# Kernel optimization log

Measured on AMD Instinct MI355X. Metric: run time of the kernel, lower is better.

## Reference

```python
import jax, jax.numpy as jnp
import numpy as np

N_NODES = 50000
N_HEDGES = 100000
E = 800000          # node->node incidences and hedge->node incidences
F_IN = 128
F_H = 64
F_OUT = 128


def setup_inputs() -> dict:
    key = jax.random.key(0)
    ks = jax.random.split(key, 10)
    node_features = jax.random.normal(ks[0], (N_NODES, F_IN), jnp.float32)
    hedge_features = jax.random.normal(ks[1], (N_HEDGES, F_H), jnp.float32)
    node_senders = jax.random.randint(ks[2], (E,), 0, N_NODES)
    node_receivers = jnp.sort(jax.random.randint(ks[3], (E,), 0, N_NODES))
    node_convolution = jax.random.uniform(ks[4], (E, 1), jnp.float32)
    hedge2node_senders = jax.random.randint(ks[5], (E,), 0, N_HEDGES)
    hedge2node_receivers = jnp.sort(jax.random.randint(ks[6], (E,), 0, N_NODES))
    hedge2node_convolution = jax.random.uniform(ks[7], (E, 1), jnp.float32)
    # eqx.nn.Linear-style uniform init: U(-1/sqrt(fan_in), 1/sqrt(fan_in))
    lim1 = 1.0 / np.sqrt(F_IN)
    lim2 = 1.0 / np.sqrt(F_H)
    W_msg = jax.random.uniform(ks[8], (F_OUT, F_IN), jnp.float32, -lim1, lim1)
    b_msg = jnp.zeros((F_OUT,), jnp.float32)
    W_scale = jax.random.uniform(ks[9], (F_OUT, F_H), jnp.float32, -lim2, lim2)
    b_scale = jnp.zeros((F_OUT,), jnp.float32)
    return dict(node_features=node_features, hedge_features=hedge_features,
                node_senders=node_senders, node_receivers=node_receivers,
                node_convolution=node_convolution,
                hedge2node_senders=hedge2node_senders,
                hedge2node_receivers=hedge2node_receivers,
                hedge2node_convolution=hedge2node_convolution,
                W_msg=W_msg, b_msg=b_msg, W_scale=W_scale, b_scale=b_scale)


def reference(node_features, hedge_features, node_senders, node_receivers,
              node_convolution, hedge2node_senders, hedge2node_receivers,
              hedge2node_convolution, W_msg, b_msg, W_scale, b_scale):
    # pipeline 1: gather node senders -> linear -> scale -> scatter-add to receivers
    sender_features = node_features[node_senders]                 # [E, F_IN]
    messages = sender_features @ W_msg.T + b_msg                  # [E, F_OUT]
    gathered_messages = jax.ops.segment_sum(
        node_convolution * messages, node_receivers, num_segments=N_NODES)
    # pipeline 2: gather hedge senders -> linear -> scale -> scatter-add to receivers
    hedge_sender_features = hedge_features[hedge2node_senders]    # [E, F_H]
    hedge_messages = hedge_sender_features @ W_scale.T + b_scale  # [E, F_OUT]
    gathered_scaling = jax.ops.segment_sum(
        hedge2node_convolution * hedge_messages, hedge2node_receivers,
        num_segments=N_NODES)
    return jnp.tanh(gathered_scaling * gathered_messages)         # [N_NODES, F_OUT]
```

## Files before the change

kernel.cpp:

```cpp
#include <hip/hip_runtime.h>

#define N_NODES   50000
#define N_HEDGES  100000
#define E_EDGES   800000
#define F_IN      128
#define F_H       64
#define F_OUT     128

typedef __attribute__((ext_vector_type(8))) short short8;
typedef __attribute__((ext_vector_type(4))) float f32x4;
typedef _Float16 half2_t __attribute__((ext_vector_type(2)));
typedef _Float16 half4_t __attribute__((ext_vector_type(4)));

__device__ __forceinline__ unsigned short f2bf(float f) {
    unsigned int u = __float_as_uint(f);
    return (unsigned short)((u + 0x7fffu + ((u >> 16) & 1u)) >> 16);
}
__device__ __forceinline__ float bf2f(unsigned short h) {
    return __uint_as_float(((unsigned int)h) << 16);
}

#define OFF_ITEMS (2 * (N_NODES + 1) + F_OUT * (F_IN + F_H))
#define OFF_B     ((OFF_ITEMS + 255) / 256)
#define CONV_NODE_F4  (N_NODES * 32)
#define CONV_HEDGE_F4 (N_HEDGES * 16)
#define CONV_B    ((CONV_NODE_F4 + CONV_HEDGE_F4 + 255) / 256)

__global__ __launch_bounds__(256)
void offsets_kernel(const int* __restrict__ recv1, const int* __restrict__ recv2,
                    int* __restrict__ offs1, int* __restrict__ offs2,
                    const float* __restrict__ Wm, const float* __restrict__ Wsc,
                    unsigned short* __restrict__ wmhi, unsigned short* __restrict__ wmlo,
                    unsigned short* __restrict__ wshi, unsigned short* __restrict__ wslo,
                    const float* __restrict__ nf, const float* __restrict__ hf,
                    _Float16* __restrict__ nfH, _Float16* __restrict__ hfH) {
    if (blockIdx.x < OFF_B) {
        int t = blockIdx.x * blockDim.x + threadIdx.x;
        const int total = N_NODES + 1;
        if (t < total) {
            int r = t, lo = 0, hi = E_EDGES;
            while (lo < hi) { int mid = (lo + hi) >> 1; if (recv1[mid] < r) lo = mid + 1; else hi = mid; }
            offs1[r] = lo;
        } else if (t < 2 * total) {
            int r = t - total, lo = 0, hi = E_EDGES;
            while (lo < hi) { int mid = (lo + hi) >> 1; if (recv2[mid] < r) lo = mid + 1; else hi = mid; }
            offs2[r] = lo;
        } else if (t < OFF_ITEMS) {
            int idx = t - 2 * total;
            if (idx < F_OUT * F_IN) {
                float f = Wm[idx];
                unsigned short h = f2bf(f);
                wmhi[idx] = h; wmlo[idx] = f2bf(f - bf2f(h));
            } else {
                int i2 = idx - F_OUT * F_IN;
                float f = Wsc[i2];
                unsigned short h = f2bf(f);
                wshi[i2] = h; wslo[i2] = f2bf(f - bf2f(h));
            }
        }
    } else {
        int idx = (blockIdx.x - OFF_B) * 256 + threadIdx.x;
        if (idx < CONV_NODE_F4) {
            float4 v = *(const float4*)(nf + (size_t)idx * 4);
            half4_t h = { (_Float16)v.x, (_Float16)v.y, (_Float16)v.z, (_Float16)v.w };
            *(half4_t*)(nfH + (size_t)idx * 4) = h;
        } else {
            int i2 = idx - CONV_NODE_F4;
            if (i2 < CONV_HEDGE_F4) {
                float4 v = *(const float4*)(hf + (size_t)i2 * 4);
                half4_t h = { (_Float16)v.x, (_Float16)v.y, (_Float16)v.z, (_Float16)v.w };
                *(half4_t*)(hfH + (size_t)i2 * 4) = h;
            }
        }
    }
}

__global__ __launch_bounds__(256)
void gather_fused(const _Float16* __restrict__ nfH, const _Float16* __restrict__ hfH,
                  const int* __restrict__ snd1, const float* __restrict__ cv1,
                  const int* __restrict__ o1,
                  const int* __restrict__ snd2, const float* __restrict__ cv2,
                  const int* __restrict__ o2,
                  char* a1pack, char* __restrict__ a2pack,
                  float* __restrict__ cs1o, float* __restrict__ cs2o) {
    const int lane = threadIdx.x & 63;
    const int wid  = threadIdx.x >> 6;

    if (blockIdx.x < N_NODES / 4) {
        const int node = blockIdx.x * 4 + wid;
        const int s = o1[node], e = o1[node + 1];
        float a0 = 0.f, a1 = 0.f, b0 = 0.f, b1 = 0.f, csA = 0.f, csB = 0.f;
        const _Float16* base = nfH + lane * 2;
        int i = s;
        for (; i + 8 <= e; i += 8) {
            int   s0 = snd1[i],   s1 = snd1[i+1], s2 = snd1[i+2], s3 = snd1[i+3];
            int   s4 = snd1[i+4], s5 = snd1[i+5], s6 = snd1[i+6], s7 = snd1[i+7];
            float c0 = cv1[i],    c1 = cv1[i+1],  c2 = cv1[i+2],  c3 = cv1[i+3];
            float c4 = cv1[i+4],  c5 = cv1[i+5],  c6 = cv1[i+6],  c7 = cv1[i+7];
            half2_t v0 = *(const half2_t*)(base + (size_t)s0 * F_IN);
            half2_t v1 = *(const half2_t*)(base + (size_t)s1 * F_IN);
            half2_t v2 = *(const half2_t*)(base + (size_t)s2 * F_IN);
            half2_t v3 = *(const half2_t*)(base + (size_t)s3 * F_IN);
            half2_t v4 = *(const half2_t*)(base + (size_t)s4 * F_IN);
            half2_t v5 = *(const half2_t*)(base + (size_t)s5 * F_IN);
            half2_t v6 = *(const half2_t*)(base + (size_t)s6 * F_IN);
            half2_t v7 = *(const half2_t*)(base + (size_t)s7 * F_IN);
            a0 += c0 * (float)v0.x; a1 += c0 * (float)v0.y;
            a0 += c1 * (float)v1.x; a1 += c1 * (float)v1.y;
            a0 += c2 * (float)v2.x; a1 += c2 * (float)v2.y;
            a0 += c3 * (float)v3.x; a1 += c3 * (float)v3.y;
            b0 += c4 * (float)v4.x; b1 += c4 * (float)v4.y;
            b0 += c5 * (float)v5.x; b1 += c5 * (float)v5.y;
            b0 += c6 * (float)v6.x; b1 += c6 * (float)v6.y;
            b0 += c7 * (float)v7.x; b1 += c7 * (float)v7.y;
            csA += c0 + c1 + c2 + c3; csB += c4 + c5 + c6 + c7;
        }
        for (; i + 4 <= e; i += 4) {
            int   s0 = snd1[i],   s1 = snd1[i+1], s2 = snd1[i+2], s3 = snd1[i+3];
            float c0 = cv1[i],    c1 = cv1[i+1],  c2 = cv1[i+2],  c3 = cv1[i+3];
            half2_t v0 = *(const half2_t*)(base + (size_t)s0 * F_IN);
            half2_t v1 = *(const half2_t*)(base + (size_t)s1 * F_IN);
            half2_t v2 = *(const half2_t*)(base + (size_t)s2 * F_IN);
            half2_t v3 = *(const half2_t*)(base + (size_t)s3 * F_IN);
            a0 += c0 * (float)v0.x; a1 += c0 * (float)v0.y;
            a0 += c1 * (float)v1.x; a1 += c1 * (float)v1.y;
            b0 += c2 * (float)v2.x; b1 += c2 * (float)v2.y;
            b0 += c3 * (float)v3.x; b1 += c3 * (float)v3.y;
            csA += c0 + c1; csB += c2 + c3;
        }
        for (; i < e; ++i) {
            int sn = snd1[i]; float c = cv1[i];
            half2_t v = *(const half2_t*)(base + (size_t)sn * F_IN);
            a0 += c * (float)v.x; a1 += c * (float)v.y; csA += c;
        }
        a0 += b0; a1 += b1;
        float cs = csA + csB;
        unsigned short h0 = f2bf(a0), h1 = f2bf(a1);
        unsigned short l0 = f2bf(a0 - bf2f(h0)), l1 = f2bf(a1 - bf2f(h1));
        unsigned int* hp = (unsigned int*)(a1pack + (size_t)node * 512);
        unsigned int* lp = (unsigned int*)(a1pack + (size_t)node * 512 + 256);
        hp[lane] = (unsigned int)h0 | ((unsigned int)h1 << 16);
        lp[lane] = (unsigned int)l0 | ((unsigned int)l1 << 16);
        if (lane == 0) cs1o[node] = cs;
    } else {
        const int node = (blockIdx.x - N_NODES / 4) * 4 + wid;
        const int s = o2[node], e = o2[node + 1];
        float a = 0.f, b = 0.f, csA = 0.f, csB = 0.f;
        const _Float16* base = hfH + lane;
        int i = s;
        for (; i + 8 <= e; i += 8) {
            int   s0 = snd2[i],   s1 = snd2[i+1], s2 = snd2[i+2], s3 = snd2[i+3];
            int   s4 = snd2[i+4], s5 = snd2[i+5], s6 = snd2[i+6], s7 = snd2[i+7];
            float c0 = cv2[i],    c1 = cv2[i+1],  c2 = cv2[i+2],  c3 = cv2[i+3];
            float c4 = cv2[i+4],  c5 = cv2[i+5],  c6 = cv2[i+6],  c7 = cv2[i+7];
            float v0 = (float)base[(size_t)s0 * F_H], v1 = (float)base[(size_t)s1 * F_H];
            float v2 = (float)base[(size_t)s2 * F_H], v3 = (float)base[(size_t)s3 * F_H];
            float v4 = (float)base[(size_t)s4 * F_H], v5 = (float)base[(size_t)s5 * F_H];
            float v6 = (float)base[(size_t)s6 * F_H], v7 = (float)base[(size_t)s7 * F_H];
            a += c0 * v0; a += c1 * v1; a += c2 * v2; a += c3 * v3;
            b += c4 * v4; b += c5 * v5; b += c6 * v6; b += c7 * v7;
            csA += c0 + c1 + c2 + c3; csB += c4 + c5 + c6 + c7;
        }
        for (; i + 4 <= e; i += 4) {
            int   s0 = snd2[i],   s1 = snd2[i+1], s2 = snd2[i+2], s3 = snd2[i+3];
            float c0 = cv2[i],    c1 = cv2[i+1],  c2 = cv2[i+2],  c3 = cv2[i+3];
            float v0 = (float)base[(size_t)s0 * F_H], v1 = (float)base[(size_t)s1 * F_H];
            float v2 = (float)base[(size_t)s2 * F_H], v3 = (float)base[(size_t)s3 * F_H];
            a += c0 * v0; a += c1 * v1; b += c2 * v2; b += c3 * v3;
            csA += c0 + c1; csB += c2 + c3;
        }
        for (; i < e; ++i) {
            int sn = snd2[i]; float c = cv2[i];
            a += c * (float)base[(size_t)sn * F_H]; csA += c;
        }
        a += b;
        float cs = csA + csB;
        unsigned short h = f2bf(a);
        unsigned short l = f2bf(a - bf2f(h));
        ((unsigned short*)(a2pack + (size_t)node * 256))[lane]       = h;
        ((unsigned short*)(a2pack + (size_t)node * 256 + 128))[lane] = l;
        if (lane == 0) cs2o[node] = cs;
    }
}

__global__ __launch_bounds__(256)
void gather_nodes_kernel(const float* __restrict__ nf, const int* __restrict__ senders,
                         const float* __restrict__ conv, const int* __restrict__ offs,
                         char* a1pack, float* __restrict__ csum_out) {
    const int lane = threadIdx.x & 63;
    const int node = blockIdx.x * 4 + (threadIdx.x >> 6);
    const int s = offs[node], e = offs[node + 1];
    float a0 = 0.f, a1 = 0.f, cs = 0.f;
    const float* base = nf + lane * 2;
    int i = s;
    for (; i + 4 <= e; i += 4) {
        int   s0 = senders[i],   s1 = senders[i+1], s2 = senders[i+2], s3 = senders[i+3];
        float c0 = conv[i],      c1 = conv[i+1],    c2 = conv[i+2],    c3 = conv[i+3];
        float2 v0 = *(const float2*)(base + s0 * F_IN);
        float2 v1 = *(const float2*)(base + s1 * F_IN);
        float2 v2 = *(const float2*)(base + s2 * F_IN);
        float2 v3 = *(const float2*)(base + s3 * F_IN);
        a0 += c0 * v0.x; a1 += c0 * v0.y;
        a0 += c1 * v1.x; a1 += c1 * v1.y;
        a0 += c2 * v2.x; a1 += c2 * v2.y;
        a0 += c3 * v3.x; a1 += c3 * v3.y;
        cs += c0 + c1 + c2 + c3;
    }
    for (; i < e; ++i) {
        int sn = senders[i]; float c = conv[i];
        float2 v = *(const float2*)(base + sn * F_IN);
        a0 += c * v.x; a1 += c * v.y; cs += c;
    }
    unsigned short h0 = f2bf(a0), h1 = f2bf(a1);
    unsigned short l0 = f2bf(a0 - bf2f(h0)), l1 = f2bf(a1 - bf2f(h1));
    unsigned int* hp = (unsigned int*)(a1pack + (size_t)node * 512);
    unsigned int* lp = (unsigned int*)(a1pack + (size_t)node * 512 + 256);
    hp[lane] = (unsigned int)h0 | ((unsigned int)h1 << 16);
    lp[lane] = (unsigned int)l0 | ((unsigned int)l1 << 16);
    if (lane == 0) csum_out[node] = cs;
}

__global__ __launch_bounds__(256)
void gather_hedges_kernel(const float* __restrict__ hf, const int* __restrict__ senders,
                          const float* __restrict__ conv, const int* __restrict__ offs,
                          char* __restrict__ a2pack, float* __restrict__ csum_out) {
    const int lane = threadIdx.x & 63;
    const int node = blockIdx.x * 4 + (threadIdx.x >> 6);
    const int s = offs[node], e = offs[node + 1];
    float a = 0.f, cs = 0.f;
    const float* base = hf + lane;
    int i = s;
    for (; i + 4 <= e; i += 4) {
        int   s0 = senders[i],   s1 = senders[i+1], s2 = senders[i+2], s3 = senders[i+3];
        float c0 = conv[i],      c1 = conv[i+1],    c2 = conv[i+2],    c3 = conv[i+3];
        float v0 = base[s0 * F_H], v1 = base[s1 * F_H];
        float v2 = base[s2 * F_H], v3 = base[s3 * F_H];
        a += c0 * v0; a += c1 * v1; a += c2 * v2; a += c3 * v3;
        cs += c0 + c1 + c2 + c3;
    }
    for (; i < e; ++i) {
        int sn = senders[i]; float c = conv[i];
        a += c * base[sn * F_H]; cs += c;
    }
    unsigned short h = f2bf(a);
    unsigned short l = f2bf(a - bf2f(h));
    ((unsigned short*)(a2pack + (size_t)node * 256))[lane]       = h;
    ((unsigned short*)(a2pack + (size_t)node * 256 + 128))[lane] = l;
    if (lane == 0) csum_out[node] = cs;
}

__global__ __launch_bounds__(256)
void gemm_tanh_kernel(const char* a1pack,
                      const char* __restrict__ a2pack,
                      const float* __restrict__ csum1, const float* __restrict__ csum2,
                      const unsigned short* __restrict__ wmhi, const unsigned short* __restrict__ wmlo,
                      const unsigned short* __restrict__ wshi, const unsigned short* __restrict__ wslo,
                      const float* __restrict__ bm, const float* __restrict__ bs,
                      float* outp) {
    __shared__ __align__(16) char sA1[16 * 512];
    __shared__ __align__(16) char sA2[16 * 256];
    __shared__ float sCs[16][2];

    const int t   = threadIdx.x;
    const int wid = t >> 6;
    const int l   = t & 63;
    const int g   = l >> 4;
    const int jl  = l & 15;

    short8 wm_h[2][4], wm_l[2][4], ws_h[2][2], ws_l[2][2];
    float bmj[2], bsj[2];
    #pragma unroll
    for (int jt = 0; jt < 2; ++jt) {
        const int j = wid * 32 + jt * 16 + jl;
        #pragma unroll
        for (int ks = 0; ks < 4; ++ks) {
            wm_h[jt][ks] = *(const short8*)(wmhi + j * F_IN + ks * 32 + g * 8);
            wm_l[jt][ks] = *(const short8*)(wmlo + j * F_IN + ks * 32 + g * 8);
        }
        #pragma unroll
        for (int ks = 0; ks < 2; ++ks) {
            ws_h[jt][ks] = *(const short8*)(wshi + j * F_H + ks * 32 + g * 8);
            ws_l[jt][ks] = *(const short8*)(wslo + j * F_H + ks * 32 + g * 8);
        }
        bmj[jt] = bm[j]; bsj[jt] = bs[j];
    }

    #pragma unroll 1
    for (int ns = 0; ns < 4; ++ns) {
        const int n0 = blockIdx.x * 64 + ns * 16;
        #pragma unroll
        for (int it = 0; it < 2; ++it) {
            int fi = (it << 8) + t;
            int ci = fi & 31, row = fi >> 5;
            int nsrc = min(n0 + row, N_NODES - 1);
            float4 v = *(const float4*)(a1pack + (size_t)nsrc * 512 + ci * 16);
            *(float4*)(sA1 + row * 512 + (((unsigned)ci << 4) ^ (((unsigned)row & 7) << 4))) = v;
        }
        {
            int ci = t & 15, row = t >> 4;
            int nsrc = min(n0 + row, N_NODES - 1);
            float4 v = *(const float4*)(a2pack + (size_t)nsrc * 256 + ci * 16);
            *(float4*)(sA2 + row * 256 + (((unsigned)ci << 4) ^ (((unsigned)row & 7) << 4))) = v;
        }
        if (t < 16)      sCs[t][0]      = csum1[min(n0 + t, N_NODES - 1)];
        else if (t < 32) sCs[t - 16][1] = csum2[min(n0 + t - 16, N_NODES - 1)];
        __syncthreads();

        short8 a1h[4], a1l[4], a2h[2], a2l[2];
        const unsigned sw = ((unsigned)jl & 7) << 4;
        #pragma unroll
        for (int ks = 0; ks < 4; ++ks) {
            unsigned cc = (((unsigned)(4 * ks + g)) << 4) ^ sw;
            a1h[ks] = *(const short8*)(sA1 + jl * 512 + cc);
            a1l[ks] = *(const short8*)(sA1 + jl * 512 + 256 + cc);
        }
        #pragma unroll
        for (int ks = 0; ks < 2; ++ks) {
            unsigned cc = (((unsigned)(4 * ks + g)) << 4) ^ sw;
            a2h[ks] = *(const short8*)(sA2 + jl * 256 + cc);
            a2l[ks] = *(const short8*)(sA2 + jl * 256 + 128 + cc);
        }

        #pragma unroll
        for (int jt = 0; jt < 2; ++jt) {
            f32x4 c1 = {0.f, 0.f, 0.f, 0.f}, c2 = {0.f, 0.f, 0.f, 0.f};
            #pragma unroll
            for (int ks = 0; ks < 4; ++ks) {
                c1 = __builtin_amdgcn_mfma_f32_16x16x32_bf16(a1h[ks], wm_h[jt][ks], c1, 0, 0, 0);
                c1 = __builtin_amdgcn_mfma_f32_16x16x32_bf16(a1h[ks], wm_l[jt][ks], c1, 0, 0, 0);
                c1 = __builtin_amdgcn_mfma_f32_16x16x32_bf16(a1l[ks], wm_h[jt][ks], c1, 0, 0, 0);
            }
            #pragma unroll
            for (int ks = 0; ks < 2; ++ks) {
                c2 = __builtin_amdgcn_mfma_f32_16x16x32_bf16(a2h[ks], ws_h[jt][ks], c2, 0, 0, 0);
                c2 = __builtin_amdgcn_mfma_f32_16x16x32_bf16(a2h[ks], ws_l[jt][ks], c2, 0, 0, 0);
                c2 = __builtin_amdgcn_mfma_f32_16x16x32_bf16(a2l[ks], ws_h[jt][ks], c2, 0, 0, 0);
            }
            const int j = wid * 32 + jt * 16 + jl;
            #pragma unroll
            for (int r = 0; r < 4; ++r) {
                int row  = g * 4 + r;
                int node = n0 + row;
                if (node < N_NODES) {
                    float v1 = c1[r] + sCs[row][0] * bmj[jt];
                    float v2 = c2[r] + sCs[row][1] * bsj[jt];
                    outp[(size_t)node * F_OUT + j] = tanhf(v1 * v2);
                }
            }
        }
        __syncthreads();
    }
}

extern "C" void kernel_launch(void* const* d_in, const int* in_sizes, int n_in,
                              void* d_out, int out_size, void* d_ws, size_t ws_size,
                              hipStream_t stream) {
    const float* node_features  = (const float*)d_in[0];
    const float* hedge_features = (const float*)d_in[1];
    const int*   node_senders   = (const int*)d_in[2];
    const int*   node_receivers = (const int*)d_in[3];
    const float* node_conv      = (const float*)d_in[4];
    const int*   h2n_senders    = (const int*)d_in[5];
    const int*   h2n_receivers  = (const int*)d_in[6];
    const float* h2n_conv       = (const float*)d_in[7];
    const float* W_msg          = (const float*)d_in[8];
    const float* b_msg          = (const float*)d_in[9];
    const float* W_scale        = (const float*)d_in[10];
    const float* b_scale        = (const float*)d_in[11];

    float* out = (float*)d_out;
    char*  ws  = (char*)d_ws;

    char*  A2pack = ws;
    float* Csum1  = (float*)(ws + 12800000);
    float* Csum2  = (float*)(ws + 13000000);
    int*   offs1  = (int*)  (ws + 13200000);
    int*   offs2  = (int*)  (ws + 13400016);
    unsigned short* wmhi = (unsigned short*)(ws + 13600032);
    unsigned short* wmlo = (unsigned short*)(ws + 13632800);
    unsigned short* wshi = (unsigned short*)(ws + 13665568);
    unsigned short* wslo = (unsigned short*)(ws + 13681952);
    _Float16* nfH = (_Float16*)(ws + 13698560);
    _Float16* hfH = (_Float16*)(ws + 26498560);
    const size_t WS_NEED_FAST = 39298560;
    char*  A1pack = (char*)d_out;

    const bool fast = (ws_size >= WS_NEED_FAST);

    if (fast) {
        offsets_kernel<<<OFF_B + CONV_B, 256, 0, stream>>>(
            node_receivers, h2n_receivers, offs1, offs2,
            W_msg, W_scale, wmhi, wmlo, wshi, wslo,
            node_features, hedge_features, nfH, hfH);
        gather_fused<<<2 * (N_NODES / 4), 256, 0, stream>>>(
            nfH, hfH,
            node_senders, node_conv, offs1,
            h2n_senders, h2n_conv, offs2,
            A1pack, A2pack, Csum1, Csum2);
    } else {
        offsets_kernel<<<OFF_B, 256, 0, stream>>>(
            node_receivers, h2n_receivers, offs1, offs2,
            W_msg, W_scale, wmhi, wmlo, wshi, wslo,
            node_features, hedge_features, nfH, hfH);
        gather_nodes_kernel<<<N_NODES / 4, 256, 0, stream>>>(
            node_features, node_senders, node_conv, offs1, A1pack, Csum1);
        gather_hedges_kernel<<<N_NODES / 4, 256, 0, stream>>>(
            hedge_features, h2n_senders, h2n_conv, offs2, A2pack, Csum2);
    }

    gemm_tanh_kernel<<<(N_NODES + 63) / 64, 256, 0, stream>>>(
        A1pack, A2pack, Csum1, Csum2, wmhi, wmlo, wshi, wslo,
        b_msg, b_scale, out);
}
```

Before: 113.3 us.

## Fuse segment gathers with MFMA GEMM and tanh in one kernel

Result: slower. 132.7 us (+17.2%).

```diff
diff --git a/kernel.cpp b/kernel.cpp
--- a/kernel.cpp
+++ b/kernel.cpp
@@ -75,19 +75,26 @@
     }
 }
 
-__global__ __launch_bounds__(256)
-void gather_fused(const _Float16* __restrict__ nfH, const _Float16* __restrict__ hfH,
-                  const int* __restrict__ snd1, const float* __restrict__ cv1,
-                  const int* __restrict__ o1,
-                  const int* __restrict__ snd2, const float* __restrict__ cv2,
-                  const int* __restrict__ o2,
-                  char* a1pack, char* __restrict__ a2pack,
-                  float* __restrict__ cs1o, float* __restrict__ cs2o) {
-    const int lane = threadIdx.x & 63;
-    const int wid  = threadIdx.x >> 6;
-
-    if (blockIdx.x < N_NODES / 4) {
-        const int node = blockIdx.x * 4 + wid;
+__global__ __launch_bounds__(1024)
+void fused_gather_gemm(const _Float16* __restrict__ nfH, const _Float16* __restrict__ hfH,
+                       const int* __restrict__ snd1, const float* __restrict__ cv1,
+                       const int* __restrict__ o1,
+                       const int* __restrict__ snd2, const float* __restrict__ cv2,
+                       const int* __restrict__ o2,
+                       const unsigned short* __restrict__ wmhi, const unsigned short* __restrict__ wmlo,
+                       const unsigned short* __restrict__ wshi, const unsigned short* __restrict__ wslo,
+                       const float* __restrict__ bm, const float* __restrict__ bs,
+                       float* __restrict__ outp) {
+    __shared__ __align__(16) char sA1[16 * 512];
+    __shared__ __align__(16) char sA2[16 * 256];
+    __shared__ float sCs[16][2];
+
+    const int t    = threadIdx.x;
+    const int wid  = t >> 6;
+    const int lane = t & 63;
+    const int node = blockIdx.x * 16 + wid;
+
+    {
         const int s = o1[node], e = o1[node + 1];
         float a0 = 0.f, a1 = 0.f, b0 = 0.f, b1 = 0.f, csA = 0.f, csB = 0.f;
         const _Float16* base = nfH + lane * 2;
@@ -134,16 +141,17 @@
             a0 += c * (float)v.x; a1 += c * (float)v.y; csA += c;
         }
         a0 += b0; a1 += b1;
-        float cs = csA + csB;
         unsigned short h0 = f2bf(a0), h1 = f2bf(a1);
         unsigned short l0 = f2bf(a0 - bf2f(h0)), l1 = f2bf(a1 - bf2f(h1));
-        unsigned int* hp = (unsigned int*)(a1pack + (size_t)node * 512);
-        unsigned int* lp = (unsigned int*)(a1pack + (size_t)node * 512 + 256);
-        hp[lane] = (unsigned int)h0 | ((unsigned int)h1 << 16);
-        lp[lane] = (unsigned int)l0 | ((unsigned int)l1 << 16);
-        if (lane == 0) cs1o[node] = cs;
-    } else {
-        const int node = (blockIdx.x - N_NODES / 4) * 4 + wid;
+        unsigned int hi = (unsigned int)h0 | ((unsigned int)h1 << 16);
+        unsigned int lo = (unsigned int)l0 | ((unsigned int)l1 << 16);
+        unsigned off = ((unsigned)(lane * 4)) ^ (((unsigned)wid & 7) << 4);
+        *(unsigned int*)(sA1 + wid * 512 + off)       = hi;
+        *(unsigned int*)(sA1 + wid * 512 + 256 + off) = lo;
+        if (lane == 0) sCs[wid][0] = csA + csB;
+    }
+
+    {
         const int s = o2[node], e = o2[node + 1];
         float a = 0.f, b = 0.f, csA = 0.f, csB = 0.f;
         const _Float16* base = hfH + lane;
@@ -174,181 +182,62 @@
             a += c * (float)base[(size_t)sn * F_H]; csA += c;
         }
         a += b;
-        float cs = csA + csB;
         unsigned short h = f2bf(a);
         unsigned short l = f2bf(a - bf2f(h));
-        ((unsigned short*)(a2pack + (size_t)node * 256))[lane]       = h;
-        ((unsigned short*)(a2pack + (size_t)node * 256 + 128))[lane] = l;
-        if (lane == 0) cs2o[node] = cs;
-    }
-}
-
-__global__ __launch_bounds__(256)
-void gather_nodes_kernel(const float* __restrict__ nf, const int* __restrict__ senders,
-                         const float* __restrict__ conv, const int* __restrict__ offs,
-                         char* a1pack, float* __restrict__ csum_out) {
-    const int lane = threadIdx.x & 63;
-    const int node = blockIdx.x * 4 + (threadIdx.x >> 6);
-    const int s = offs[node], e = offs[node + 1];
-    float a0 = 0.f, a1 = 0.f, cs = 0.f;
-    const float* base = nf + lane * 2;
-    int i = s;
-    for (; i + 4 <= e; i += 4) {
-        int   s0 = senders[i],   s1 = senders[i+1], s2 = senders[i+2], s3 = senders[i+3];
-        float c0 = conv[i],      c1 = conv[i+1],    c2 = conv[i+2],    c3 = conv[i+3];
-        float2 v0 = *(const float2*)(base + s0 * F_IN);
-        float2 v1 = *(const float2*)(base + s1 * F_IN);
-        float2 v2 = *(const float2*)(base + s2 * F_IN);
-        float2 v3 = *(const float2*)(base + s3 * F_IN);
-        a0 += c0 * v0.x; a1 += c0 * v0.y;
-        a0 += c1 * v1.x; a1 += c1 * v1.y;
-        a0 += c2 * v2.x; a1 += c2 * v2.y;
-        a0 += c3 * v3.x; a1 += c3 * v3.y;
-        cs += c0 + c1 + c2 + c3;
-    }
-    for (; i < e; ++i) {
-        int sn = senders[i]; float c = conv[i];
-        float2 v = *(const float2*)(base + sn * F_IN);
-        a0 += c * v.x; a1 += c * v.y; cs += c;
-    }
-    unsigned short h0 = f2bf(a0), h1 = f2bf(a1);
-    unsigned short l0 = f2bf(a0 - bf2f(h0)), l1 = f2bf(a1 - bf2f(h1));
-    unsigned int* hp = (unsigned int*)(a1pack + (size_t)node * 512);
-    unsigned int* lp = (unsigned int*)(a1pack + (size_t)node * 512 + 256);
-    hp[lane] = (unsigned int)h0 | ((unsigned int)h1 << 16);
-    lp[lane] = (unsigned int)l0 | ((unsigned int)l1 << 16);
-    if (lane == 0) csum_out[node] = cs;
-}
-
-__global__ __launch_bounds__(256)
-void gather_hedges_kernel(const float* __restrict__ hf, const int* __restrict__ senders,
-                          const float* __restrict__ conv, const int* __restrict__ offs,
-                          char* __restrict__ a2pack, float* __restrict__ csum_out) {
-    const int lane = threadIdx.x & 63;
-    const int node = blockIdx.x * 4 + (threadIdx.x >> 6);
-    const int s = offs[node], e = offs[node + 1];
-    float a = 0.f, cs = 0.f;
-    const float* base = hf + lane;
-    int i = s;
-    for (; i + 4 <= e; i += 4) {
-        int   s0 = senders[i],   s1 = senders[i+1], s2 = senders[i+2], s3 = senders[i+3];
-        float c0 = conv[i],      c1 = conv[i+1],    c2 = conv[i+2],    c3 = conv[i+3];
-        float v0 = base[s0 * F_H], v1 = base[s1 * F_H];
-        float v2 = base[s2 * F_H], v3 = base[s3 * F_H];
-        a += c0 * v0; a += c1 * v1; a += c2 * v2; a += c3 * v3;
-        cs += c0 + c1 + c2 + c3;
-    }
-    for (; i < e; ++i) {
-        int sn = senders[i]; float c = conv[i];
-        a += c * base[sn * F_H]; cs += c;
-    }
-    unsigned short h = f2bf(a);
-    unsigned short l = f2bf(a - bf2f(h));
-    ((unsigned short*)(a2pack + (size_t)node * 256))[lane]       = h;
-    ((unsigned short*)(a2pack + (size_t)node * 256 + 128))[lane] = l;
-    if (lane == 0) csum_out[node] = cs;
-}
-
-__global__ __launch_bounds__(256)
-void gemm_tanh_kernel(const char* a1pack,
-                      const char* __restrict__ a2pack,
-                      const float* __restrict__ csum1, const float* __restrict__ csum2,
-                      const unsigned short* __restrict__ wmhi, const unsigned short* __restrict__ wmlo,
-                      const unsigned short* __restrict__ wshi, const unsigned short* __restrict__ wslo,
-                      const float* __restrict__ bm, const float* __restrict__ bs,
-                      float* outp) {
-    __shared__ __align__(16) char sA1[16 * 512];
-    __shared__ __align__(16) char sA2[16 * 256];
-    __shared__ float sCs[16][2];
-
-    const int t   = threadIdx.x;
-    const int wid = t >> 6;
-    const int l   = t & 63;
-    const int g   = l >> 4;
-    const int jl  = l & 15;
-
-    short8 wm_h[2][4], wm_l[2][4], ws_h[2][2], ws_l[2][2];
-    float bmj[2], bsj[2];
-    #pragma unroll
-    for (int jt = 0; jt < 2; ++jt) {
-        const int j = wid * 32 + jt * 16 + jl;
-        #pragma unroll
-        for (int ks = 0; ks < 4; ++ks) {
-            wm_h[jt][ks] = *(const short8*)(wmhi + j * F_IN + ks * 32 + g * 8);
-            wm_l[jt][ks] = *(const short8*)(wmlo + j * F_IN + ks * 32 + g * 8);
-        }
-        #pragma unroll
-        for (int ks = 0; ks < 2; ++ks) {
-            ws_h[jt][ks] = *(const short8*)(wshi + j * F_H + ks * 32 + g * 8);
-            ws_l[jt][ks] = *(const short8*)(wslo + j * F_H + ks * 32 + g * 8);
-        }
-        bmj[jt] = bm[j]; bsj[jt] = bs[j];
-    }
-
-    #pragma unroll 1
-    for (int ns = 0; ns < 4; ++ns) {
-        const int n0 = blockIdx.x * 64 + ns * 16;
-        #pragma unroll
-        for (int it = 0; it < 2; ++it) {
-            int fi = (it << 8) + t;
-            int ci = fi & 31, row = fi >> 5;
-            int nsrc = min(n0 + row, N_NODES - 1);
-            float4 v = *(const float4*)(a1pack + (size_t)nsrc * 512 + ci * 16);
-            *(float4*)(sA1 + row * 512 + (((unsigned)ci << 4) ^ (((unsigned)row & 7) << 4))) = v;
-        }
-        {
-            int ci = t & 15, row = t >> 4;
-            int nsrc = min(n0 + row, N_NODES - 1);
-            float4 v = *(const float4*)(a2pack + (size_t)nsrc * 256 + ci * 16);
-            *(float4*)(sA2 + row * 256 + (((unsigned)ci << 4) ^ (((unsigned)row & 7) << 4))) = v;
-        }
-        if (t < 16)      sCs[t][0]      = csum1[min(n0 + t, N_NODES - 1)];
-        else if (t < 32) sCs[t - 16][1] = csum2[min(n0 + t - 16, N_NODES - 1)];
-        __syncthreads();
-
-        short8 a1h[4], a1l[4], a2h[2], a2l[2];
-        const unsigned sw = ((unsigned)jl & 7) << 4;
-        #pragma unroll
-        for (int ks = 0; ks < 4; ++ks) {
-            unsigned cc = (((unsigned)(4 * ks + g)) << 4) ^ sw;
-            a1h[ks] = *(const short8*)(sA1 + jl * 512 + cc);
-            a1l[ks] = *(const short8*)(sA1 + jl * 512 + 256 + cc);
-        }
-        #pragma unroll
-        for (int ks = 0; ks < 2; ++ks) {
-            unsigned cc = (((unsigned)(4 * ks + g)) << 4) ^ sw;
-            a2h[ks] = *(const short8*)(sA2 + jl * 256 + cc);
-            a2l[ks] = *(const short8*)(sA2 + jl * 256 + 128 + cc);
-        }
-
-        #pragma unroll
-        for (int jt = 0; jt < 2; ++jt) {
-            f32x4 c1 = {0.f, 0.f, 0.f, 0.f}, c2 = {0.f, 0.f, 0.f, 0.f};
-            #pragma unroll
-            for (int ks = 0; ks < 4; ++ks) {
-                c1 = __builtin_amdgcn_mfma_f32_16x16x32_bf16(a1h[ks], wm_h[jt][ks], c1, 0, 0, 0);
-                c1 = __builtin_amdgcn_mfma_f32_16x16x32_bf16(a1h[ks], wm_l[jt][ks], c1, 0, 0, 0);
-                c1 = __builtin_amdgcn_mfma_f32_16x16x32_bf16(a1l[ks], wm_h[jt][ks], c1, 0, 0, 0);
-            }
-            #pragma unroll
-            for (int ks = 0; ks < 2; ++ks) {
-                c2 = __builtin_amdgcn_mfma_f32_16x16x32_bf16(a2h[ks], ws_h[jt][ks], c2, 0, 0, 0);
-                c2 = __builtin_amdgcn_mfma_f32_16x16x32_bf16(a2h[ks], ws_l[jt][ks], c2, 0, 0, 0);
-                c2 = __builtin_amdgcn_mfma_f32_16x16x32_bf16(a2l[ks], ws_h[jt][ks], c2, 0, 0, 0);
-            }
-            const int j = wid * 32 + jt * 16 + jl;
-            #pragma unroll
-            for (int r = 0; r < 4; ++r) {
-                int row  = g * 4 + r;
-                int node = n0 + row;
-                if (node < N_NODES) {
-                    float v1 = c1[r] + sCs[row][0] * bmj[jt];
-                    float v2 = c2[r] + sCs[row][1] * bsj[jt];
-                    outp[(size_t)node * F_OUT + j] = tanhf(v1 * v2);
-                }
-            }
-        }
-        __syncthreads();
+        unsigned off = ((unsigned)(lane * 2)) ^ (((unsigned)wid & 7) << 4);
+        *(unsigned short*)(sA2 + wid * 256 + off)       = h;
+        *(unsigned short*)(sA2 + wid * 256 + 128 + off) = l;
+        if (lane == 0) sCs[wid][1] = csA + csB;
+    }
+
+    __syncthreads();
+    if (wid >= 8) return;
+
+    const int g  = lane >> 4;
+    const int jl = lane & 15;
+    const int j  = wid * 16 + jl;
+
+    short8 wm_h[4], wm_l[4], ws_h[2], ws_l[2];
+    #pragma unroll
+    for (int ks = 0; ks < 4; ++ks) {
+        wm_h[ks] = *(const short8*)(wmhi + j * F_IN + ks * 32 + g * 8);
+        wm_l[ks] = *(const short8*)(wmlo + j * F_IN + ks * 32 + g * 8);
+    }
+    #pragma unroll
+    for (int ks = 0; ks < 2; ++ks) {
+        ws_h[ks] = *(const short8*)(wshi + j * F_H + ks * 32 + g * 8);
+        ws_l[ks] = *(const short8*)(wslo + j * F_H + ks * 32 + g * 8);
+    }
+    const float bmj = bm[j], bsj = bs[j];
+
+    const unsigned sw = ((unsigned)jl & 7) << 4;
+    f32x4 c1 = {0.f, 0.f, 0.f, 0.f}, c2 = {0.f, 0.f, 0.f, 0.f};
+    #pragma unroll
+    for (int ks = 0; ks < 4; ++ks) {
+        unsigned cc = (((unsigned)(4 * ks + g)) << 4) ^ sw;
+        short8 a1h = *(const short8*)(sA1 + jl * 512 + cc);
+        short8 a1l = *(const short8*)(sA1 + jl * 512 + 256 + cc);
+        c1 = __builtin_amdgcn_mfma_f32_16x16x32_bf16(a1h, wm_h[ks], c1, 0, 0, 0);
+        c1 = __builtin_amdgcn_mfma_f32_16x16x32_bf16(a1h, wm_l[ks], c1, 0, 0, 0);
+        c1 = __builtin_amdgcn_mfma_f32_16x16x32_bf16(a1l, wm_h[ks], c1, 0, 0, 0);
+    }
+    #pragma unroll
+    for (int ks = 0; ks < 2; ++ks) {
+        unsigned cc = (((unsigned)(4 * ks + g)) << 4) ^ sw;
+        short8 a2h = *(const short8*)(sA2 + jl * 256 + cc);
+        short8 a2l = *(const short8*)(sA2 + jl * 256 + 128 + cc);
+        c2 = __builtin_amdgcn_mfma_f32_16x16x32_bf16(a2h, ws_h[ks], c2, 0, 0, 0);
+        c2 = __builtin_amdgcn_mfma_f32_16x16x32_bf16(a2h, ws_l[ks], c2, 0, 0, 0);
+        c2 = __builtin_amdgcn_mfma_f32_16x16x32_bf16(a2l, ws_h[ks], c2, 0, 0, 0);
+    }
+
+    const int n0 = blockIdx.x * 16;
+    #pragma unroll
+    for (int r = 0; r < 4; ++r) {
+        int row = g * 4 + r;
+        float v1 = c1[r] + sCs[row][0] * bmj;
+        float v2 = c2[r] + sCs[row][1] * bsj;
+        outp[(size_t)(n0 + row) * F_OUT + j] = tanhf(v1 * v2);
     }
 }
 
@@ -371,44 +260,24 @@
     float* out = (float*)d_out;
     char*  ws  = (char*)d_ws;
 
-    char*  A2pack = ws;
-    float* Csum1  = (float*)(ws + 12800000);
-    float* Csum2  = (float*)(ws + 13000000);
-    int*   offs1  = (int*)  (ws + 13200000);
-    int*   offs2  = (int*)  (ws + 13400016);
-    unsigned short* wmhi = (unsigned short*)(ws + 13600032);
-    unsigned short* wmlo = (unsigned short*)(ws + 13632800);
-    unsigned short* wshi = (unsigned short*)(ws + 13665568);
-    unsigned short* wslo = (unsigned short*)(ws + 13681952);
-    _Float16* nfH = (_Float16*)(ws + 13698560);
-    _Float16* hfH = (_Float16*)(ws + 26498560);
-    const size_t WS_NEED_FAST = 39298560;
-    char*  A1pack = (char*)d_out;
-
-    const bool fast = (ws_size >= WS_NEED_FAST);
-
-    if (fast) {
-        offsets_kernel<<<OFF_B + CONV_B, 256, 0, stream>>>(
-            node_receivers, h2n_receivers, offs1, offs2,
-            W_msg, W_scale, wmhi, wmlo, wshi, wslo,
-            node_features, hedge_features, nfH, hfH);
-        gather_fused<<<2 * (N_NODES / 4), 256, 0, stream>>>(
-            nfH, hfH,
-            node_senders, node_conv, offs1,
-            h2n_senders, h2n_conv, offs2,
-            A1pack, A2pack, Csum1, Csum2);
-    } else {
-        offsets_kernel<<<OFF_B, 256, 0, stream>>>(
-            node_receivers, h2n_receivers, offs1, offs2,
-            W_msg, W_scale, wmhi, wmlo, wshi, wslo,
-            node_features, hedge_features, nfH, hfH);
-        gather_nodes_kernel<<<N_NODES / 4, 256, 0, stream>>>(
-            node_features, node_senders, node_conv, offs1, A1pack, Csum1);
-        gather_hedges_kernel<<<N_NODES / 4, 256, 0, stream>>>(
-            hedge_features, h2n_senders, h2n_conv, offs2, A2pack, Csum2);
-    }
-
-    gemm_tanh_kernel<<<(N_NODES + 63) / 64, 256, 0, stream>>>(
-        A1pack, A2pack, Csum1, Csum2, wmhi, wmlo, wshi, wslo,
+    int*   offs1 = (int*)  (ws);
+    int*   offs2 = (int*)  (ws + 200016);
+    unsigned short* wmhi = (unsigned short*)(ws + 400032);
+    unsigned short* wmlo = (unsigned short*)(ws + 432800);
+    unsigned short* wshi = (unsigned short*)(ws + 465568);
+    unsigned short* wslo = (unsigned short*)(ws + 481952);
+    _Float16* nfH = (_Float16*)(ws + 498336);
+    _Float16* hfH = (_Float16*)(ws + 13298336);
+
+    offsets_kernel<<<OFF_B + CONV_B, 256, 0, stream>>>(
+        node_receivers, h2n_receivers, offs1, offs2,
+        W_msg, W_scale, wmhi, wmlo, wshi, wslo,
+        node_features, hedge_features, nfH, hfH);
+
+    fused_gather_gemm<<<N_NODES / 16, 1024, 0, stream>>>(
+        nfH, hfH,
+        node_senders, node_conv, offs1,
+        h2n_senders, h2n_conv, offs2,
+        wmhi, wmlo, wshi, wslo,
         b_msg, b_scale, out);
 }
```
